# Optimization experiments

Hardware: AMD Instinct MI355X
Metric: run time of the kernel (lower is better)

## Reference

```python
import jax, jax.numpy as jnp
import numpy as np

B, C, H, W = 4, 256, 64, 64
C8 = C // 8

def setup_inputs() -> dict:
    key = jax.random.key(0)
    ks = jax.random.split(key, 8)
    s = 1.0 / np.sqrt(C)
    return {
        "x": jax.random.normal(ks[0], (B, C, H, W), dtype=jnp.float32),
        "wq": jax.random.normal(ks[1], (C8, C), dtype=jnp.float32) * s,
        "bq": jax.random.normal(ks[2], (C8,), dtype=jnp.float32) * 0.01,
        "wk": jax.random.normal(ks[3], (C8, C), dtype=jnp.float32) * s,
        "bk": jax.random.normal(ks[4], (C8,), dtype=jnp.float32) * 0.01,
        "wv": jax.random.normal(ks[5], (C, C), dtype=jnp.float32) * s,
        "bv": jax.random.normal(ks[6], (C,), dtype=jnp.float32) * 0.01,
        "gamma": jax.random.normal(ks[7], (1,), dtype=jnp.float32) * 0.1,
    }

def reference(x, wq, bq, wk, bk, wv, bv, gamma):
    b, c, h, w = x.shape
    n = h * w
    xf = x.reshape(b, c, n)                       # [B,C,N]
    # 1x1 convs == per-pixel linear projections
    q = jnp.einsum('dc,bcn->bdn', wq, xf) + bq[None, :, None]   # [B,C8,N]
    k = jnp.einsum('dc,bcn->bdn', wk, xf) + bk[None, :, None]   # [B,C8,N]
    v = jnp.einsum('dc,bcn->bdn', wv, xf) + bv[None, :, None]   # [B,C,N]
    energy = jnp.einsum('bdi,bdj->bij', q, k)     # [B,N,N], i=query, j=key
    attn = jax.nn.softmax(energy, axis=-1)
    out = jnp.einsum('bcj,bij->bci', v, attn)     # [B,C,N]
    out = out.reshape(b, c, h, w)
    return gamma * out + x
```

## Files before the change

### kernel.cpp

```cpp
#include <hip/hip_runtime.h>
#include <math.h>

#define BATCH 4
#define CH    256
#define CQK   32
#define NPIX  4096
#define NT    32
#define LOG2E 1.4426950408889634f

typedef __attribute__((ext_vector_type(8))) short short8;
typedef __attribute__((ext_vector_type(4))) float f32x4;

static __device__ __forceinline__ unsigned short f2bf(float f) {
    unsigned u = __builtin_bit_cast(unsigned, f);
    u = (u + 0x7fffu + ((u >> 16) & 1u)) >> 16;
    return (unsigned short)u;
}
static __device__ __forceinline__ float bf2f(unsigned short s) {
    unsigned u = ((unsigned)s) << 16;
    return __builtin_bit_cast(float, u);
}
static __device__ __forceinline__ float exp2_fast(float x) {
    float r; asm("v_exp_f32 %0, %1" : "=v"(r) : "v"(x)); return r;
}
static __device__ __forceinline__ unsigned cvt_pk_bf16(float lo, float hi) {
    unsigned r; asm("v_cvt_pk_bf16_f32 %0, %1, %2" : "=v"(r) : "v"(lo), "v"(hi)); return r;
}

__global__ __launch_bounds__(256) void wcvt_kernel(
    const float* __restrict__ wq, const float* __restrict__ wk,
    const float* __restrict__ wv,
    unsigned short* __restrict__ Wh)
{
    int idx = blockIdx.x * 256 + threadIdx.x;
    int r = idx >> 8, c = idx & 255;
    float f;
    if (r < 32)       f = wq[r * 256 + c] * LOG2E;
    else if (r < 64)  f = wk[(r - 32) * 256 + c];
    else              f = wv[(r - 64) * 256 + c];
    Wh[idx] = f2bf(f);
}

__global__ __launch_bounds__(256) void qkv_kernel(
    const float* __restrict__ x,
    const float* __restrict__ bq, const float* __restrict__ bk,
    const float* __restrict__ bv,
    const unsigned short* __restrict__ Wh,
    unsigned short* __restrict__ Qh, unsigned short* __restrict__ Kh,
    unsigned short* __restrict__ Vb)
{
    __shared__ __align__(16) char Xh[64 * 512];

    const int b  = blockIdx.y;
    const int n0 = blockIdx.x * 64;
    const int t  = threadIdx.x;

    #pragma unroll
    for (int rep = 0; rep < 8; ++rep) {
        int idx = rep * 256 + t;
        int cp = idx >> 4, n4 = idx & 15;
        int c = cp * 2;
        float4 a4 = *(const float4*)&x[((size_t)b * CH + c) * NPIX + n0 + n4 * 4];
        float4 b4 = *(const float4*)&x[((size_t)b * CH + c + 1) * NPIX + n0 + n4 * 4];
        #pragma unroll
        for (int u = 0; u < 4; ++u) {
            int n = n4 * 4 + u;
            int off = n * 512 + (((c >> 3) * 16) ^ ((n & 7) << 4)) + (c & 7) * 2;
            *(unsigned*)(Xh + off) =
                (unsigned)f2bf((&a4.x)[u]) | ((unsigned)f2bf((&b4.x)[u]) << 16);
        }
    }
    __syncthreads();

    const int w = t >> 6, l = t & 63, g = l >> 4, m = l & 15;

    for (int dt = 0; dt < 5; ++dt) {
        const int d0 = w * 80 + dt * 16;

        short8 wh[8];
        #pragma unroll
        for (int ks = 0; ks < 8; ++ks) {
            size_t off = (size_t)(d0 + m) * 256 + ks * 32 + g * 8;
            wh[ks] = __builtin_bit_cast(short8, *(const uint4*)&Wh[off]);
        }

        f32x4 acc[4];
        #pragma unroll
        for (int nt = 0; nt < 4; ++nt) acc[nt] = (f32x4){0.f, 0.f, 0.f, 0.f};
        #pragma unroll
        for (int nt = 0; nt < 4; ++nt) {
            const int n = nt * 16 + m;
            #pragma unroll
            for (int ks = 0; ks < 8; ++ks) {
                int off = n * 512 + (((ks * 4 + g) * 16) ^ ((n & 7) << 4));
                short8 xh = __builtin_bit_cast(short8, *(const uint4*)(Xh + off));
                acc[nt] = __builtin_amdgcn_mfma_f32_16x16x32_bf16(wh[ks], xh, acc[nt], 0, 0, 0);
            }
        }

        int kind;
        float4 bias;
        if (d0 < 32)      { kind = 0; bias = *(const float4*)&bq[d0 + g * 4];
                            bias.x *= LOG2E; bias.y *= LOG2E; bias.z *= LOG2E; bias.w *= LOG2E; }
        else if (d0 < 64) { kind = 1; bias = *(const float4*)&bk[d0 - 32 + g * 4]; }
        else              { kind = 2; bias = *(const float4*)&bv[d0 - 64 + g * 4]; }

        #pragma unroll
        for (int nt = 0; nt < 4; ++nt) {
            const int n = n0 + nt * 16 + m;
            if (kind == 2) {
                const int c0 = d0 - 64;
                #pragma unroll
                for (int r = 0; r < 4; ++r) {
                    float val = acc[nt][r] + (&bias.x)[r];
                    Vb[((size_t)b * CH + c0 + g * 4 + r) * NPIX + n] = f2bf(val);
                }
            } else {
                unsigned short hs[4];
                #pragma unroll
                for (int r = 0; r < 4; ++r)
                    hs[r] = f2bf(acc[nt][r] + (&bias.x)[r]);
                const int dcol = (d0 & 31) + g * 4;
                const size_t base = ((size_t)b * NPIX + n) * CQK + dcol;
                uint2 uh;
                uh.x = (unsigned)hs[0] | ((unsigned)hs[1] << 16);
                uh.y = (unsigned)hs[2] | ((unsigned)hs[3] << 16);
                if (kind == 0) *(uint2*)&Qh[base] = uh;
                else           *(uint2*)&Kh[base] = uh;
            }
        }
    }
}


#define CONS_STEP(JT, PF) do {                                                 \
    const int _jb   = ((JT) - 1) * 128;                                        \
    const int _pidx = ((JT) & 1) ^ 1;                                          \
    const char* pb = (const char*)Pbuf[_pidx];                                 \
    float ff[4];                                                               \
    _Pragma("unroll")                                                          \
    for (int f = 0; f < 4; ++f) ff[f] = sFac[_pidx][f * 16 + m];               \
    uint4 vB[8];                                                               \
    _Pragma("unroll")                                                          \
    for (int cf = 0; cf < 4; ++cf) {                                           \
        vB[cf * 2]     = *(const uint4*)&vrow[cf][_jb + 64 + g * 8];           \
        vB[cf * 2 + 1] = *(const uint4*)&vrow[cf][_jb + 96 + g * 8];           \
    }                                                                          \
    short8 pf[4][2];                                                           \
    _Pragma("unroll")                                                          \
    for (int f = 0; f < 4; ++f)                                                \
        _Pragma("unroll")                                                      \
        for (int k2 = 0; k2 < 2; ++k2)                                         \
            pf[f][k2] = __builtin_bit_cast(short8, *(const uint4*)(pb +        \
                (f * 16 + m) * 256 + ((k2 * 64 + g * 16) ^ (m << 4))));        \
    if (!__all(ff[0] == 1.f && ff[1] == 1.f && ff[2] == 1.f && ff[3] == 1.f)) { \
        _Pragma("unroll")                                                      \
        for (int cf = 0; cf < 4; ++cf)                                         \
            _Pragma("unroll")                                                  \
            for (int f = 0; f < 4; ++f) acc[cf][f] *= ff[f];                   \
    }                                                                          \
    _Pragma("unroll")                                                          \
    for (int cf = 0; cf < 4; ++cf) {                                           \
        short8 v0 = __builtin_bit_cast(short8, vAc[cf * 2]);                   \
        short8 v1 = __builtin_bit_cast(short8, vAc[cf * 2 + 1]);               \
        _Pragma("unroll")                                                      \
        for (int f = 0; f < 4; ++f) {                                          \
            f32x4 a = acc[cf][f];                                              \
            a = __builtin_amdgcn_mfma_f32_16x16x32_bf16(v0, pf[f][0], a, 0, 0, 0); \
            a = __builtin_amdgcn_mfma_f32_16x16x32_bf16(v1, pf[f][1], a, 0, 0, 0); \
            acc[cf][f] = a;                                                    \
        }                                                                      \
    }                                                                          \
    if (PF) {                                                                  \
        _Pragma("unroll")                                                      \
        for (int cf = 0; cf < 4; ++cf) {                                       \
            vAc[cf * 2]     = *(const uint4*)&vrow[cf][_jb + 128 + g * 8];     \
            vAc[cf * 2 + 1] = *(const uint4*)&vrow[cf][_jb + 160 + g * 8];     \
        }                                                                      \
    }                                                                          \
    short8 pg[4][2];                                                           \
    _Pragma("unroll")                                                          \
    for (int f = 0; f < 4; ++f)                                                \
        _Pragma("unroll")                                                      \
        for (int k2 = 0; k2 < 2; ++k2)                                         \
            pg[f][k2] = __builtin_bit_cast(short8, *(const uint4*)(pb +        \
                (f * 16 + m) * 256 + (((k2 + 2) * 64 + g * 16) ^ (m << 4))));  \
    _Pragma("unroll")                                                          \
    for (int cf = 0; cf < 4; ++cf) {                                           \
        short8 v0 = __builtin_bit_cast(short8, vB[cf * 2]);                    \
        short8 v1 = __builtin_bit_cast(short8, vB[cf * 2 + 1]);                \
        _Pragma("unroll")                                                      \
        for (int f = 0; f < 4; ++f) {                                          \
            f32x4 a = acc[cf][f];                                              \
            a = __builtin_amdgcn_mfma_f32_16x16x32_bf16(v0, pg[f][0], a, 0, 0, 0); \
            a = __builtin_amdgcn_mfma_f32_16x16x32_bf16(v1, pg[f][1], a, 0, 0, 0); \
            acc[cf][f] = a;                                                    \
        }                                                                      \
    }                                                                          \
} while (0)

__global__ __launch_bounds__(512, 2) void attn_kernel(
    const unsigned short* __restrict__ Qh, const unsigned short* __restrict__ Kh,
    const unsigned short* __restrict__ Vb,
    const float* __restrict__ x, const float* __restrict__ gamma,
    float* __restrict__ out)
{
    __shared__ __align__(16) char Ksw[2][8192];
    __shared__ __align__(16) uint4 Pbuf[2][1024];
    __shared__ float sFac[2][64];
    __shared__ float sL[64];

    const int bid = blockIdx.x;
    const int b   = (bid & 7) >> 1;
    const int it  = (bid >> 3) + ((bid & 1) << 5);
    const int i0  = it * 64;

    const int t   = threadIdx.x;
    const int wv8 = t >> 6;
    const bool isProd = (wv8 < 4);
    const int w   = wv8 & 3;
    const int l   = t & 63, g = l >> 4, m = l & 15;
    const int irow = w * 16 + m;

    {
        int sj = t >> 2, sq = t & 3;
        int wr = sj * 64 + ((sq * 16) ^ (((sj >> 1) & 3) << 4));
        *(uint4*)&Ksw[0][wr] =
            *(const uint4*)&Kh[((size_t)b * NPIX + sj) * CQK + sq * 8];
    }

    short8 qh = {};
    float m_run = -1e30f, l_run = 0.f;
    if (isProd) {
        const int iq = i0 + irow;
        qh = __builtin_bit_cast(short8, *(const uint4*)&Qh[((size_t)b * NPIX + iq) * CQK + g * 8]);
    }

    f32x4 acc[4][4];
    #pragma unroll
    for (int cf = 0; cf < 4; ++cf)
        #pragma unroll
        for (int f = 0; f < 4; ++f) acc[cf][f] = (f32x4){0.f, 0.f, 0.f, 0.f};
    const unsigned short* vrow[4];
    uint4 vAc[8];
    size_t kpf_base = 0;
    int kwr0 = 0;
    if (!isProd) {
        #pragma unroll
        for (int cf = 0; cf < 4; ++cf)
            vrow[cf] = Vb + ((size_t)b * CH + w * 64 + cf * 16 + m) * NPIX;
        const int t2  = t & 255;
        const int sj0 = t2 >> 2, sq0 = t2 & 3;
        kpf_base = ((size_t)b * NPIX + sj0) * CQK + sq0 * 8;
        kwr0 = sj0 * 64 + ((sq0 * 16) ^ (((sj0 >> 1) & 3) << 4));
        #pragma unroll
        for (int cf = 0; cf < 4; ++cf) {
            vAc[cf * 2]     = *(const uint4*)&vrow[cf][g * 8];
            vAc[cf * 2 + 1] = *(const uint4*)&vrow[cf][32 + g * 8];
        }
    }

    __syncthreads();

    for (int jt = 0; jt < NT; ++jt) {
        const int idx = jt & 1;

        if (isProd) {
            f32x4 sv[8];
            #pragma unroll
            for (int jf = 0; jf < 8; ++jf) {
                short8 kh8 = __builtin_bit_cast(short8,
                    *(const uint4*)&Ksw[idx][jf * 1024 + m * 64 +
                        ((g * 16) ^ (((m >> 1) & 3) << 4))]);
                f32x4 s = (f32x4){0.f, 0.f, 0.f, 0.f};
                s = __builtin_amdgcn_mfma_f32_16x16x32_bf16(kh8, qh, s, 0, 0, 0);
                sv[jf] = s;
            }

            float s32[32];
            #pragma unroll
            for (int jf = 0; jf < 8; ++jf)
                #pragma unroll
                for (int r = 0; r < 4; ++r) s32[jf * 4 + r] = sv[jf][r];

            float mx[16];
            #pragma unroll
            for (int k = 0; k < 16; ++k) mx[k] = fmaxf(s32[k], s32[k + 16]);
            #pragma unroll
            for (int k = 0; k < 8; ++k) mx[k] = fmaxf(mx[k], mx[k + 8]);
            #pragma unroll
            for (int k = 0; k < 4; ++k) mx[k] = fmaxf(mx[k], mx[k + 4]);
            float tmax = fmaxf(fmaxf(mx[0], mx[2]), fmaxf(mx[1], mx[3]));

            float fac = 1.0f;
            if (!__all(tmax <= m_run + 11.5f)) {
                float tc = fmaxf(tmax, __shfl_xor(tmax, 16));
                tc = fmaxf(tc, __shfl_xor(tc, 32));
                float mt = fmaxf(m_run, tc);
                fac = exp2_fast(m_run - mt);
                m_run = mt;
            }

            float p[32];
            #pragma unroll
            for (int k = 0; k < 32; ++k) p[k] = exp2_fast(s32[k] - m_run);
            float sm[16];
            #pragma unroll
            for (int k = 0; k < 16; ++k) sm[k] = p[k] + p[k + 16];
            #pragma unroll
            for (int k = 0; k < 8; ++k) sm[k] = sm[k] + sm[k + 8];
            #pragma unroll
            for (int k = 0; k < 4; ++k) sm[k] = sm[k] + sm[k + 4];
            float tsum = (sm[0] + sm[2]) + (sm[1] + sm[3]);
            tsum += __shfl_xor(tsum, 16);
            tsum += __shfl_xor(tsum, 32);
            l_run = l_run * fac + tsum;
            if (g == 0) sFac[idx][irow] = fac;

            char* pb = (char*)Pbuf[idx];
            #pragma unroll
            for (int jf = 0; jf < 8; ++jf) {
                uint2 u;
                u.x = cvt_pk_bf16(p[jf * 4 + 0], p[jf * 4 + 1]);
                u.y = cvt_pk_bf16(p[jf * 4 + 2], p[jf * 4 + 3]);
                *(uint2*)(pb + irow * 256 + ((jf * 32 + g * 8) ^ (m << 4))) = u;
            }
        } else {
            const bool doK = (jt < NT - 1);
            uint4 pk0, pk1;
            if (doK) {
                const size_t rb = kpf_base + (size_t)((jt + 1) * 128) * CQK;
                pk0 = *(const uint4*)&Kh[rb];
                pk1 = *(const uint4*)&Kh[rb + 2048];
            }

            if (jt >= 1) CONS_STEP(jt, true);

            if (doK) {
                *(uint4*)&Ksw[idx ^ 1][kwr0] = pk0;
                *(uint4*)&Ksw[idx ^ 1][kwr0 + 4096] = pk1;
            }
        }

        __syncthreads();
    }

    if (isProd) {
        if (g == 0) sL[irow] = l_run;
    }
    __syncthreads();
    if (!isProd) {
        CONS_STEP(NT, false);
        const float gm = gamma[0];
        #pragma unroll
        for (int f = 0; f < 4; ++f) {
            float linv = 1.0f / sL[f * 16 + m];
            #pragma unroll
            for (int cf = 0; cf < 4; ++cf) {
                #pragma unroll
                for (int r = 0; r < 4; ++r) {
                    int c = w * 64 + cf * 16 + g * 4 + r;
                    size_t o = ((size_t)b * CH + c) * NPIX + i0 + f * 16 + m;
                    out[o] = gm * acc[cf][f][r] * linv + x[o];
                }
            }
        }
    }
}

extern "C" void kernel_launch(void* const* d_in, const int* in_sizes, int n_in,
                              void* d_out, int out_size, void* d_ws, size_t ws_size,
                              hipStream_t stream) {
    const float* x     = (const float*)d_in[0];
    const float* wq    = (const float*)d_in[1];
    const float* bq    = (const float*)d_in[2];
    const float* wk    = (const float*)d_in[3];
    const float* bk    = (const float*)d_in[4];
    const float* wv    = (const float*)d_in[5];
    const float* bv    = (const float*)d_in[6];
    const float* gamma = (const float*)d_in[7];
    float* out = (float*)d_out;

    unsigned short* base = (unsigned short*)d_ws;
    const size_t qk_sz = (size_t)BATCH * NPIX * CQK;
    unsigned short* Qh = base;
    unsigned short* Kh = Qh + qk_sz;
    unsigned short* Vb = Kh + qk_sz;
    unsigned short* Wh = Vb + (size_t)BATCH * CH * NPIX;

    wcvt_kernel<<<320, 256, 0, stream>>>(wq, wk, wv, Wh);
    qkv_kernel<<<dim3(64, 4), 256, 0, stream>>>(x, bq, bk, bv, Wh, Qh, Kh, Vb);
    attn_kernel<<<256, 512, 0, stream>>>(Qh, Kh, Vb, x, gamma, out);
}
```

Measured before the change: 89.45 us.

## Split PV consumer work across 8 waves with split-K reduction through LDS

```diff
diff --git a/kernel.cpp b/kernel.cpp
--- a/kernel.cpp
+++ b/kernel.cpp
@@ -133,18 +133,18 @@
 }
 
 
-#define CONS_STEP(JT, PF) do {                                                 \
-    const int _jb   = ((JT) - 1) * 128;                                        \
+#define CONS_SPLIT(JT) do {                                                    \
+    const int _jb   = ((JT) - 1) * 128 + ch * 64;                              \
     const int _pidx = ((JT) & 1) ^ 1;                                          \
     const char* pb = (const char*)Pbuf[_pidx];                                 \
     float ff[4];                                                               \
     _Pragma("unroll")                                                          \
     for (int f = 0; f < 4; ++f) ff[f] = sFac[_pidx][f * 16 + m];               \
-    uint4 vB[8];                                                               \
+    uint4 vA[8];                                                               \
     _Pragma("unroll")                                                          \
     for (int cf = 0; cf < 4; ++cf) {                                           \
-        vB[cf * 2]     = *(const uint4*)&vrow[cf][_jb + 64 + g * 8];           \
-        vB[cf * 2 + 1] = *(const uint4*)&vrow[cf][_jb + 96 + g * 8];           \
+        vA[cf * 2]     = *(const uint4*)&vrow[cf][_jb + g * 8];                \
+        vA[cf * 2 + 1] = *(const uint4*)&vrow[cf][_jb + 32 + g * 8];           \
     }                                                                          \
     short8 pf[4][2];                                                           \
     _Pragma("unroll")                                                          \
@@ -152,7 +152,7 @@
         _Pragma("unroll")                                                      \
         for (int k2 = 0; k2 < 2; ++k2)                                         \
             pf[f][k2] = __builtin_bit_cast(short8, *(const uint4*)(pb +        \
-                (f * 16 + m) * 256 + ((k2 * 64 + g * 16) ^ (m << 4))));        \
+                (f * 16 + m) * 256 + ((((ch * 2 + k2) * 64) + g * 16) ^ (m << 4)))); \
     if (!__all(ff[0] == 1.f && ff[1] == 1.f && ff[2] == 1.f && ff[3] == 1.f)) { \
         _Pragma("unroll")                                                      \
         for (int cf = 0; cf < 4; ++cf)                                         \
@@ -161,8 +161,8 @@
     }                                                                          \
     _Pragma("unroll")                                                          \
     for (int cf = 0; cf < 4; ++cf) {                                           \
-        short8 v0 = __builtin_bit_cast(short8, vAc[cf * 2]);                   \
-        short8 v1 = __builtin_bit_cast(short8, vAc[cf * 2 + 1]);               \
+        short8 v0 = __builtin_bit_cast(short8, vA[cf * 2]);                    \
+        short8 v1 = __builtin_bit_cast(short8, vA[cf * 2 + 1]);                \
         _Pragma("unroll")                                                      \
         for (int f = 0; f < 4; ++f) {                                          \
             f32x4 a = acc[cf][f];                                              \
@@ -171,35 +171,9 @@
             acc[cf][f] = a;                                                    \
         }                                                                      \
     }                                                                          \
-    if (PF) {                                                                  \
-        _Pragma("unroll")                                                      \
-        for (int cf = 0; cf < 4; ++cf) {                                       \
-            vAc[cf * 2]     = *(const uint4*)&vrow[cf][_jb + 128 + g * 8];     \
-            vAc[cf * 2 + 1] = *(const uint4*)&vrow[cf][_jb + 160 + g * 8];     \
-        }                                                                      \
-    }                                                                          \
-    short8 pg[4][2];                                                           \
-    _Pragma("unroll")                                                          \
-    for (int f = 0; f < 4; ++f)                                                \
-        _Pragma("unroll")                                                      \
-        for (int k2 = 0; k2 < 2; ++k2)                                         \
-            pg[f][k2] = __builtin_bit_cast(short8, *(const uint4*)(pb +        \
-                (f * 16 + m) * 256 + (((k2 + 2) * 64 + g * 16) ^ (m << 4))));  \
-    _Pragma("unroll")                                                          \
-    for (int cf = 0; cf < 4; ++cf) {                                           \
-        short8 v0 = __builtin_bit_cast(short8, vB[cf * 2]);                    \
-        short8 v1 = __builtin_bit_cast(short8, vB[cf * 2 + 1]);                \
-        _Pragma("unroll")                                                      \
-        for (int f = 0; f < 4; ++f) {                                          \
-            f32x4 a = acc[cf][f];                                              \
-            a = __builtin_amdgcn_mfma_f32_16x16x32_bf16(v0, pg[f][0], a, 0, 0, 0); \
-            a = __builtin_amdgcn_mfma_f32_16x16x32_bf16(v1, pg[f][1], a, 0, 0, 0); \
-            acc[cf][f] = a;                                                    \
-        }                                                                      \
-    }                                                                          \
 } while (0)
 
-__global__ __launch_bounds__(512, 2) void attn_kernel(
+__global__ __launch_bounds__(768, 3) void attn_kernel(
     const unsigned short* __restrict__ Qh, const unsigned short* __restrict__ Kh,
     const unsigned short* __restrict__ Vb,
     const float* __restrict__ x, const float* __restrict__ gamma,
@@ -215,14 +189,17 @@
     const int it  = (bid >> 3) + ((bid & 1) << 5);
     const int i0  = it * 64;
 
-    const int t   = threadIdx.x;
-    const int wv8 = t >> 6;
-    const bool isProd = (wv8 < 4);
-    const int w   = wv8 & 3;
-    const int l   = t & 63, g = l >> 4, m = l & 15;
+    const int t    = threadIdx.x;
+    const int wv12 = t >> 6;
+    const bool isProd = (wv12 < 4);
+    const int w    = wv12 & 3;
+    const int cw   = wv12 - 4;
+    const int cg   = cw & 3;
+    const int ch   = cw >> 2;
+    const int l    = t & 63, g = l >> 4, m = l & 15;
     const int irow = w * 16 + m;
 
-    {
+    if (t < 512) {
         int sj = t >> 2, sq = t & 3;
         int wr = sj * 64 + ((sq * 16) ^ (((sj >> 1) & 3) << 4));
         *(uint4*)&Ksw[0][wr] =
@@ -242,22 +219,16 @@
         #pragma unroll
         for (int f = 0; f < 4; ++f) acc[cf][f] = (f32x4){0.f, 0.f, 0.f, 0.f};
     const unsigned short* vrow[4];
-    uint4 vAc[8];
     size_t kpf_base = 0;
     int kwr0 = 0;
     if (!isProd) {
         #pragma unroll
         for (int cf = 0; cf < 4; ++cf)
-            vrow[cf] = Vb + ((size_t)b * CH + w * 64 + cf * 16 + m) * NPIX;
-        const int t2  = t & 255;
+            vrow[cf] = Vb + ((size_t)b * CH + cg * 64 + cf * 16 + m) * NPIX;
+        const int t2  = t - 256;
         const int sj0 = t2 >> 2, sq0 = t2 & 3;
         kpf_base = ((size_t)b * NPIX + sj0) * CQK + sq0 * 8;
         kwr0 = sj0 * 64 + ((sq0 * 16) ^ (((sj0 >> 1) & 3) << 4));
-        #pragma unroll
-        for (int cf = 0; cf < 4; ++cf) {
-            vAc[cf * 2]     = *(const uint4*)&vrow[cf][g * 8];
-            vAc[cf * 2 + 1] = *(const uint4*)&vrow[cf][32 + g * 8];
-        }
     }
 
     __syncthreads();
@@ -327,41 +298,64 @@
             }
         } else {
             const bool doK = (jt < NT - 1);
-            uint4 pk0, pk1;
-            if (doK) {
-                const size_t rb = kpf_base + (size_t)((jt + 1) * 128) * CQK;
-                pk0 = *(const uint4*)&Kh[rb];
-                pk1 = *(const uint4*)&Kh[rb + 2048];
-            }
-
-            if (jt >= 1) CONS_STEP(jt, true);
-
-            if (doK) {
+            uint4 pk0;
+            if (doK)
+                pk0 = *(const uint4*)&Kh[kpf_base + (size_t)((jt + 1) * 128) * CQK];
+
+            if (jt >= 1) CONS_SPLIT(jt);
+
+            if (doK)
                 *(uint4*)&Ksw[idx ^ 1][kwr0] = pk0;
-                *(uint4*)&Ksw[idx ^ 1][kwr0 + 4096] = pk1;
-            }
         }
 
         __syncthreads();
     }
 
-    if (isProd) {
-        if (g == 0) sL[irow] = l_run;
-    }
+    if (isProd && g == 0) sL[irow] = l_run;
     __syncthreads();
-    if (!isProd) {
-        CONS_STEP(NT, false);
+    if (!isProd) CONS_SPLIT(NT);
+
+    float* const Red = (float*)&Pbuf[0][0];
+    #pragma unroll
+    for (int rnd = 0; rnd < 2; ++rnd) {
+        if (!isProd && ch == 1) {
+            #pragma unroll
+            for (int cfl = 0; cfl < 2; ++cfl) {
+                #pragma unroll
+                for (int f = 0; f < 4; ++f) {
+                    int e4 = cfl * 4 + f;
+                    int off = cg * 2048 + l * 32 + 4 * (e4 ^ (l & 7));
+                    *(f32x4*)&Red[off] = acc[rnd * 2 + cfl][f];
+                }
+            }
+        }
+        __syncthreads();
+        if (!isProd && ch == 0) {
+            #pragma unroll
+            for (int cfl = 0; cfl < 2; ++cfl) {
+                #pragma unroll
+                for (int f = 0; f < 4; ++f) {
+                    int e4 = cfl * 4 + f;
+                    int off = cg * 2048 + l * 32 + 4 * (e4 ^ (l & 7));
+                    acc[rnd * 2 + cfl][f] += *(const f32x4*)&Red[off];
+                }
+            }
+        }
+        __syncthreads();
+    }
+
+    if (!isProd && ch == 0) {
         const float gm = gamma[0];
         #pragma unroll
         for (int f = 0; f < 4; ++f) {
-            float linv = 1.0f / sL[f * 16 + m];
+            float linv = gm / sL[f * 16 + m];
             #pragma unroll
             for (int cf = 0; cf < 4; ++cf) {
                 #pragma unroll
                 for (int r = 0; r < 4; ++r) {
-                    int c = w * 64 + cf * 16 + g * 4 + r;
+                    int c = cg * 64 + cf * 16 + g * 4 + r;
                     size_t o = ((size_t)b * CH + c) * NPIX + i0 + f * 16 + m;
-                    out[o] = gm * acc[cf][f][r] * linv + x[o];
+                    out[o] = acc[cf][f][r] * linv + x[o];
                 }
             }
         }
@@ -390,5 +384,5 @@
 
     wcvt_kernel<<<320, 256, 0, stream>>>(wq, wk, wv, Wh);
     qkv_kernel<<<dim3(64, 4), 256, 0, stream>>>(x, bq, bk, bv, Wh, Qh, Kh, Vb);
-    attn_kernel<<<256, 512, 0, stream>>>(Qh, Kh, Vb, x, gamma, out);
-}
+    attn_kernel<<<256, 768, 0, stream>>>(Qh, Kh, Vb, x, gamma, out);
+}
```

After: 121.5 us. 1.36x slower.
